# Kernel tuning notes

Measured on AMD Instinct MI355X. Metric: run time of the kernel, lower is better.

Reference implementation:

```python
import jax, jax.numpy as jnp
import numpy as np

N = 100000
E = 1600000
D_IN, H1, H2 = 64, 128, 64
ATT = 32


def _mean_aggregate(feat, src, dst, num_nodes):
    # gather source features per edge, scatter-sum to destinations, divide by in-degree
    summed = jax.ops.segment_sum(feat[src], dst, num_segments=num_nodes)  # [N, d]
    deg = jax.ops.segment_sum(jnp.ones((src.shape[0],), feat.dtype), dst, num_segments=num_nodes)
    return summed / jnp.maximum(deg, 1.0)[:, None]


def setup_inputs() -> dict:
    key = jax.random.key(0)
    ks = jax.random.split(key, 16)
    x = jax.random.normal(ks[0], (N, D_IN), dtype=jnp.float32)
    edge_index = jax.random.randint(ks[1], (2, E), 0, N, dtype=jnp.int64)

    def lin(k, fan_in, fan_out):
        bound = 1.0 / np.sqrt(fan_in)
        return jax.random.uniform(k, (fan_in, fan_out), jnp.float32, -bound, bound)

    params = {
        'W1_l': lin(ks[2], D_IN, H1), 'W1_r': lin(ks[3], D_IN, H1),
        'b1': jnp.zeros((H1,), jnp.float32),
        'W2_l': lin(ks[4], H1, H2), 'W2_r': lin(ks[5], H1, H2),
        'b2': jnp.zeros((H2,), jnp.float32),
        'Wa': lin(ks[6], H2, ATT), 'ba': jnp.zeros((ATT,), jnp.float32),
        'ctx': jax.random.normal(ks[7], (ATT,), jnp.float32),
        'Wc1': lin(ks[8], H2, H2 // 2), 'bc1': jnp.zeros((H2 // 2,), jnp.float32),
        'Wc2': lin(ks[9], H2 // 2, 1), 'bc2': jnp.zeros((1,), jnp.float32),
    }
    return {'x': x, 'edge_index': edge_index, **params}


def reference(x, edge_index, W1_l, W1_r, b1, W2_l, W2_r, b2, Wa, ba, ctx, Wc1, bc1, Wc2, bc2):
    src, dst = edge_index[0], edge_index[1]
    ionm_alerts = x[:, -1]  # [N]

    # GraphSAGE layer 1 (mean aggr): lin_l(mean_neighbors) + lin_r(x_self)
    agg1 = _mean_aggregate(x, src, dst, N)
    h = jax.nn.relu(agg1 @ W1_l + b1 + x @ W1_r)  # [N, H1]
    # F.dropout(training=False) -> identity

    # GraphSAGE layer 2
    agg2 = _mean_aggregate(h, src, dst, N)
    h = jax.nn.relu(agg2 @ W2_l + b2 + h @ W2_r)  # [N, H2]

    # attention with IONM alert boost (+0.4)
    scores = jnp.tanh(h @ Wa + ba)            # [N, ATT]
    w = scores @ ctx + ionm_alerts * 0.4       # [N]
    w = jax.nn.softmax(w, axis=0)
    h = h * w[:, None]

    pooled = jnp.mean(h, axis=0, keepdims=True)  # [1, H2]

    # classifier head (Dropout identity in eval)
    z = jax.nn.relu(pooled @ Wc1 + bc1)
    return jax.nn.sigmoid(z @ Wc2 + bc2)  # [1, 1]
```

## Files before the change

### kernel.cpp

```cpp
#include <hip/hip_runtime.h>
#include <math.h>

#define N_NODES 100000
#define E_EDGES 1600000
#define D_IN 64
#define HID1 128
#define HID2 64
#define ATT 32
#define CAP 32
#define AT_STRIDE 136
#define NRANGE 8
#define RNODES (N_NODES / NRANGE)
#define NPART 64
#define XCAST_BLOCKS ((N_NODES * 16 + 255) / 256)
#define NBLK 1024
#define EPB  1563
#define SEGCAP 384
#define SCAT2_BLOCKS 2048
#define GBLK 3125

#define SX 0.4f
#define INVSX 2.5f
#define SV 0.25f
#define INVSV 4.0f

typedef unsigned int uint32;
typedef unsigned short ushort;
typedef __attribute__((ext_vector_type(8))) short short8;
typedef __attribute__((ext_vector_type(4))) float float4v;
typedef __attribute__((ext_vector_type(2))) unsigned int uint32x2;
typedef __attribute__((ext_vector_type(4))) unsigned int uint32x4;

#define NTL(p) __builtin_nontemporal_load(&(p))

__device__ inline uint32 bf16rn(float f){ uint32 u = __float_as_uint(f); return (u + 0x7fffu + ((u >> 16) & 1u)) >> 16; }
__device__ inline uint32 packbf2(float a, float b){ return bf16rn(a) | (bf16rn(b) << 16); }

__device__ inline int swz3125(int bb){
    int x = bb & 7, k = bb >> 3;
    return (x < 5) ? x * 391 + k : 5 * 391 + (x - 5) * 390 + k;
}

#if __has_builtin(__builtin_amdgcn_sdot8)
#define HW_SDOT8 1
#endif

__device__ inline uint32 q4(float v, float inv){
    float n = rintf(v * inv);
    n = fminf(fmaxf(n, -8.f), 7.f);
    return (uint32)((int)n) & 15u;
}

__device__ inline void dec4i(uint32 w, int sh, int& a0, int& a1, int& a2, int& a3){
    a0 += ((int)(w << (28 - sh))) >> 28;
    a1 += ((int)(w << (24 - sh))) >> 28;
    a2 += ((int)(w << (20 - sh))) >> 28;
    a3 += ((int)(w << (16 - sh))) >> 28;
}

__global__ void k_mega(const float* __restrict__ x,
                       const int* __restrict__ src, const int* __restrict__ dst,
                       const float* __restrict__ W1l, const float* __restrict__ W1r,
                       const float* __restrict__ W2l, const float* __restrict__ W2r,
                       uint32* __restrict__ xb, uint32* __restrict__ xq4,
                       uint32* __restrict__ vq4, float* __restrict__ alertv,
                       ushort* __restrict__ wt1g, ushort* __restrict__ wt2g,
                       uint32x2* __restrict__ qu, int* __restrict__ qlen){
    int b = blockIdx.x, t = threadIdx.x;
    if (b < XCAST_BLOCKS){
        int i = b * 256 + t;
        if (i < N_NODES * 16){
            float4v v = NTL(((const float4v*)x)[i]);
            xb[2 * i]     = packbf2(v.x, v.y);
            xb[2 * i + 1] = packbf2(v.z, v.w);
            ((ushort*)xq4)[i] = (ushort)(q4(v.x, INVSX) | (q4(v.y, INVSX) << 4)
                              | (q4(v.z, INVSX) << 8) | (q4(v.w, INVSX) << 12));
            if ((i & 15) == 15) alertv[i >> 4] = v.w;
        }
        return;
    }
    if (b < XCAST_BLOCKS + 2){
        int sub = b - XCAST_BLOCKS;
        ushort* dstp = (sub == 0) ? wt1g : wt2g;
        for (int idx = t; idx < 128 * 128; idx += 256){
            int nn = idx >> 7, kk = idx & 127;
            float v;
            if (sub == 0) v = (kk < 64) ? W1l[kk * 128 + nn] : W1r[(kk - 64) * 128 + nn];
            else          v = (nn < 64) ? W2l[kk * 64 + nn]  : W2r[kk * 64 + (nn - 64)];
            dstp[nn * 128 + kk] = (ushort)bf16rn(v);
        }
        if (sub == 0){
            if (t < 8) xq4[(size_t)N_NODES * 8 + t] = 0u;
            else if (t < 16) vq4[(size_t)N_NODES * 8 + (t - 8)] = 0u;
        }
        return;
    }
    int blk = b - (XCAST_BLOCKS + 2);
    __shared__ int tails[NRANGE];
    if (t < NRANGE) tails[t] = 0;
    __syncthreads();
    int lane = t & 63;
    int base = blk * EPB;
    int end  = min(base + EPB, E_EDGES);
    for (int i0 = base; i0 < end; i0 += 256){
        int i = i0 + t;
        bool v = (i < end);
        int d = 0, s = 0, r = NRANGE;
        if (v){
            d = NTL(dst[i]);
            s = NTL(src[i]);
            r = (int)((uint32)d / (uint32)RNODES);
        }
        int mybase = 0, myoff = 0;
        #pragma unroll
        for (int k = 0; k < NRANGE; k++){
            unsigned long long mk = __ballot(r == k);
            if (r == k){
                int leader = (int)__ffsll((unsigned long long)mk) - 1;
                int nk = (int)__popcll(mk);
                int bse = 0;
                if (lane == leader) bse = atomicAdd(&tails[k], nk);
                bse = __shfl(bse, leader, 64);
                mybase = bse;
                myoff  = (int)__popcll(mk & ((lane == 63) ? 0x7fffffffffffffffull
                                                          : ((1ull << lane) - 1ull)));
            }
        }
        if (v){
            int pos = mybase + myoff;
            if (pos < SEGCAP)
                qu[(size_t)(blk * NRANGE + r) * SEGCAP + pos] = (uint32x2){(uint32)d, (uint32)s};
        }
    }
    __syncthreads();
    if (t < NRANGE) qlen[blk * NRANGE + t] = min(tails[t], SEGCAP);
}

__global__ __launch_bounds__(256) void k_scat2(const uint32x2* __restrict__ qu,
                                               const int* __restrict__ qlen,
                                               int* __restrict__ cnt, int* __restrict__ ssrc){
    int bb = blockIdx.x, t = threadIdx.x;
    int r = bb & (NRANGE - 1);
    int sidx = bb >> 3;
    #pragma unroll 1
    for (int k = 0; k < NBLK / (SCAT2_BLOCKS / NRANGE); k++){
        int seg = sidx * 4 + k;
        int qi = seg * NRANGE + r;
        int len = min(qlen[qi], SEGCAP);
        const uint32x2* qp = &qu[(size_t)qi * SEGCAP];
        for (int i = t; i < len; i += 256){
            uint32x2 pr = NTL(qp[i]);
            int d = (int)pr.x, s = (int)pr.y;
            int pos = atomicAdd(&cnt[d], 1);
            if (pos < CAP) ssrc[d * CAP + pos] = s;
        }
    }
}

__device__ inline void gather8_i4(const uint32* __restrict__ tab4,
                                  const int* __restrict__ ssrc,
                                  const int* __restrict__ cnt,
                                  int n0, int lane,
                                  int acc[8][4], int cct[8]){
    int q = lane >> 4, p = lane & 15;
    int dw = p >> 1, sh = (p & 1) << 4;
#ifdef HW_SDOT8
    uint32 sel0 = 1u << sh;
#endif
    int nn = n0 + (lane & 7);
    int ccl_ = cnt[nn];
    int cc[8];
    #pragma unroll
    for (int j = 0; j < 8; j++){
        int c = __shfl(ccl_, j, 64);
        cct[j] = c;
        cc[j] = min(c, CAP);
    }
    #pragma unroll
    for (int j = 0; j < 8; j++){ acc[j][0] = acc[j][1] = acc[j][2] = acc[j][3] = 0; }
    int cmax = 0;
    #pragma unroll
    for (int j = 0; j < 8; j++) cmax = max(cmax, cc[j]);
    if (cmax == 0) return;
    int se[8];
    #pragma unroll
    for (int j = 0; j < 8; j++)
        se[j] = (lane < cc[j]) ? NTL(ssrc[(n0 + j) * CAP + lane]) : N_NODES;

    uint32 w[4][8];
    #pragma unroll
    for (int g = 0; g < 4; g++){
        #pragma unroll
        for (int j = 0; j < 8; j++){
            int s = __shfl(se[j], g * 4 + q, 64);
            w[g][j] = tab4[(uint32)s * 8u + dw];
        }
    }
    #pragma unroll
    for (int g = 0; g < 4; g++){
        #pragma unroll
        for (int j = 0; j < 8; j++){
#ifdef HW_SDOT8
            acc[j][0] = __builtin_amdgcn_sdot8((int)w[g][j], (int)sel0,         acc[j][0], false);
            acc[j][1] = __builtin_amdgcn_sdot8((int)w[g][j], (int)(sel0 << 4),  acc[j][1], false);
            acc[j][2] = __builtin_amdgcn_sdot8((int)w[g][j], (int)(sel0 << 8),  acc[j][2], false);
            acc[j][3] = __builtin_amdgcn_sdot8((int)w[g][j], (int)(sel0 << 12), acc[j][3], false);
#else
            dec4i(w[g][j], sh, acc[j][0], acc[j][1], acc[j][2], acc[j][3]);
#endif
        }
    }
    if (cmax > 16){
        #pragma unroll
        for (int g = 0; g < 4; g++){
            #pragma unroll
            for (int j = 0; j < 8; j++){
                int s = __shfl(se[j], 16 + g * 4 + q, 64);
                w[g][j] = tab4[(uint32)s * 8u + dw];
            }
        }
        #pragma unroll
        for (int g = 0; g < 4; g++){
            #pragma unroll
            for (int j = 0; j < 8; j++){
#ifdef HW_SDOT8
                acc[j][0] = __builtin_amdgcn_sdot8((int)w[g][j], (int)sel0,         acc[j][0], false);
                acc[j][1] = __builtin_amdgcn_sdot8((int)w[g][j], (int)(sel0 << 4),  acc[j][1], false);
                acc[j][2] = __builtin_amdgcn_sdot8((int)w[g][j], (int)(sel0 << 8),  acc[j][2], false);
                acc[j][3] = __builtin_amdgcn_sdot8((int)w[g][j], (int)(sel0 << 12), acc[j][3], false);
#else
                dec4i(w[g][j], sh, acc[j][0], acc[j][1], acc[j][2], acc[j][3]);
#endif
            }
        }
    }
    #pragma unroll
    for (int j = 0; j < 8; j++){
        acc[j][0] += __shfl_xor(acc[j][0], 16, 64); acc[j][1] += __shfl_xor(acc[j][1], 16, 64);
        acc[j][2] += __shfl_xor(acc[j][2], 16, 64); acc[j][3] += __shfl_xor(acc[j][3], 16, 64);
        acc[j][0] += __shfl_xor(acc[j][0], 32, 64); acc[j][1] += __shfl_xor(acc[j][1], 32, 64);
        acc[j][2] += __shfl_xor(acc[j][2], 32, 64); acc[j][3] += __shfl_xor(acc[j][3], 32, 64);
    }
}

__device__ inline float inv_deg(int c){ return 1.f / fmaxf(fminf((float)c, (float)CAP), 1.f); }

__global__ __launch_bounds__(256) void k_gather(
    const uint32* __restrict__ tab4,
    const int* __restrict__ ssrc, const int* __restrict__ cnt,
    float scl, uint32* __restrict__ aggb, float* __restrict__ pzero){
    int t = threadIdx.x, wave = t >> 6, lane = t & 63;
    if (pzero != nullptr && blockIdx.x == 0){
        for (int i = t; i < NPART * 65; i += 256) pzero[i] = 0.f;
    }
    int nb0 = swz3125((int)blockIdx.x) * 32;
    int n0 = nb0 + wave * 8;
    int acc[8][4]; int cct[8];
    gather8_i4(tab4, ssrc, cnt, n0, lane, acc, cct);
    int p = lane & 15;
    if (lane < 16){
        #pragma unroll
        for (int j = 0; j < 8; j++){
            float f = scl * inv_deg(cct[j]);
            uint2 o;
            o.x = packbf2((float)acc[j][0] * f, (float)acc[j][1] * f);
            o.y = packbf2((float)acc[j][2] * f, (float)acc[j][3] * f);
            *(uint2*)&aggb[(size_t)(n0 + j) * 32 + 2 * p] = o;
        }
    }
}

__global__ __launch_bounds__(256) void k_mm(
    const uint32* __restrict__ aggb, const uint32* __restrict__ xb,
    const ushort* __restrict__ wt1g, const ushort* __restrict__ wt2g,
    const float* __restrict__ b1, const float* __restrict__ b2,
    uint32* __restrict__ vq4, ushort* __restrict__ r2b){
    __shared__ ushort smem[2 * 32 * AT_STRIDE];
    ushort* at  = smem;
    ushort* at2 = smem + 32 * AT_STRIDE;
    float* vstage = (float*)smem;
    int t = threadIdx.x, wave = t >> 6, lane = t & 63;
    int nb0 = swz3125((int)blockIdx.x) * 32;

    int m0 = t >> 3, ch = t & 7;
    uint4 aval = *(const uint4*)&aggb[(size_t)(nb0 + m0) * 32 + ch * 4];
    uint4 xval = *(const uint4*)&xb[(size_t)(nb0 + m0) * 32 + ch * 4];
    *(uint4*)((uint32*)(at + m0 * AT_STRIDE) + ch * 4) = aval;
    *(uint4*)((uint32*)(at + m0 * AT_STRIDE + 64) + ch * 4) = xval;
    __syncthreads();

    int cidx = lane & 15, quad = lane >> 4;
    int mt = wave >> 1;
    int nbase = (wave & 1) * 64;
    float4v c[4];
    #pragma unroll
    for (int nt = 0; nt < 4; nt++) c[nt] = (float4v){0.f,0.f,0.f,0.f};
    #pragma unroll
    for (int kt = 0; kt < 4; kt++){
        short8 a = *(short8*)(at + ((mt * 16 + cidx) * AT_STRIDE + kt * 32 + quad * 8));
        #pragma unroll
        for (int nt = 0; nt < 4; nt++){
            short8 b = *(const short8*)(wt1g + ((nbase + nt * 16 + cidx) * 128 + kt * 32 + quad * 8));
            c[nt] = __builtin_amdgcn_mfma_f32_16x16x32_bf16(a, b, c[nt], 0, 0, 0);
        }
    }
    #pragma unroll
    for (int nt = 0; nt < 4; nt++){
        float bb = b1[nbase + nt * 16 + cidx];
        #pragma unroll
        for (int i = 0; i < 4; i++){
            int row = quad * 4 + i;
            at2[(mt * 16 + row) * AT_STRIDE + nbase + nt * 16 + cidx] =
                (ushort)bf16rn(fmaxf(c[nt][i] + bb, 0.f));
        }
    }
    __syncthreads();
    #pragma unroll
    for (int nt = 0; nt < 4; nt++) c[nt] = (float4v){0.f,0.f,0.f,0.f};
    #pragma unroll
    for (int kt = 0; kt < 4; kt++){
        short8 a = *(short8*)(at2 + ((mt * 16 + cidx) * AT_STRIDE + kt * 32 + quad * 8));
        #pragma unroll
        for (int nt = 0; nt < 4; nt++){
            short8 b = *(const short8*)(wt2g + ((nbase + nt * 16 + cidx) * 128 + kt * 32 + quad * 8));
            c[nt] = __builtin_amdgcn_mfma_f32_16x16x32_bf16(a, b, c[nt], 0, 0, 0);
        }
    }
    if (nbase == 0){
        #pragma unroll
        for (int nt = 0; nt < 4; nt++){
            #pragma unroll
            for (int i = 0; i < 4; i++){
                int row = quad * 4 + i;
                vstage[(mt * 16 + row) * 65 + nt * 16 + cidx] = c[nt][i];
            }
        }
    } else {
        #pragma unroll
        for (int nt = 0; nt < 4; nt++){
            float bb = b2[nt * 16 + cidx];
            #pragma unroll
            for (int i = 0; i < 4; i++){
                int row = quad * 4 + i;
                size_t node = nb0 + mt * 16 + row;
                r2b[node * 64 + nt * 16 + cidx] = (ushort)bf16rn(c[nt][i] + bb);
            }
        }
    }
    __syncthreads();
    {
        int m = t >> 3, u = t & 7;
        float f0 = vstage[m * 65 + 8 * u],     f1 = vstage[m * 65 + 8 * u + 1];
        float f2 = vstage[m * 65 + 8 * u + 2], f3 = vstage[m * 65 + 8 * u + 3];
        float f4 = vstage[m * 65 + 8 * u + 4], f5 = vstage[m * 65 + 8 * u + 5];
        float f6 = vstage[m * 65 + 8 * u + 6], f7 = vstage[m * 65 + 8 * u + 7];
        vq4[(size_t)(nb0 + m) * 8 + u] =
              q4(f0, INVSV)        | (q4(f1, INVSV) << 4)  | (q4(f2, INVSV) << 8)
            | (q4(f3, INVSV) << 12)| (q4(f4, INVSV) << 16) | (q4(f5, INVSV) << 20)
            | (q4(f6, INVSV) << 24)| (q4(f7, INVSV) << 28);
    }
}

__device__ inline float bf16lo(uint32 u){ return __uint_as_float(u << 16); }
__device__ inline float bf16hi(uint32 u){ return __uint_as_float(u & 0xffff0000u); }

__global__ __launch_bounds__(256) void k_att(
    const float* __restrict__ alertv, const uint32* __restrict__ aggvb,
    const ushort* __restrict__ r2b,
    const float* __restrict__ Wa, const float* __restrict__ ba, const float* __restrict__ ctx,
    float* __restrict__ pooledP, float* __restrict__ Zpart){
    __shared__ float sh2[32][68];
    __shared__ float sew[32];
    __shared__ float sp[4][64];
    int t = threadIdx.x;
    int bn0 = swz3125((int)blockIdx.x) * 32;
    int m0 = t >> 3, ch = t & 7;
    {
        size_t nj = bn0 + m0;
        uint4 av = *(const uint4*)&aggvb[nj * 32 + ch * 4];
        uint4 rr = *(const uint4*)&r2b[nj * 64 + ch * 8];
        float4v h0, h1;
        h0.x = fmaxf(bf16lo(av.x) + bf16lo(rr.x), 0.f);
        h0.y = fmaxf(bf16hi(av.x) + bf16hi(rr.x), 0.f);
        h0.z = fmaxf(bf16lo(av.y) + bf16lo(rr.y), 0.f);
        h0.w = fmaxf(bf16hi(av.y) + bf16hi(rr.y), 0.f);
        h1.x = fmaxf(bf16lo(av.z) + bf16lo(rr.z), 0.f);
        h1.y = fmaxf(bf16hi(av.z) + bf16hi(rr.z), 0.f);
        h1.z = fmaxf(bf16lo(av.w) + bf16lo(rr.w), 0.f);
        h1.w = fmaxf(bf16hi(av.w) + bf16hi(rr.w), 0.f);
        *(float4v*)&sh2[m0][8 * ch]     = h0;
        *(float4v*)&sh2[m0][8 * ch + 4] = h1;
    }
    __syncthreads();
    int node = t >> 3;
    int c0 = (t & 7) * 4;
    float s0 = ba[c0], s1 = ba[c0 + 1], s2 = ba[c0 + 2], s3 = ba[c0 + 3];
    #pragma unroll 8
    for (int j = 0; j < 64; j++){
        float hv = sh2[node][j];
        s0 += hv * Wa[j * ATT + c0];
        s1 += hv * Wa[j * ATT + c0 + 1];
        s2 += hv * Wa[j * ATT + c0 + 2];
        s3 += hv * Wa[j * ATT + c0 + 3];
    }
    float pa = tanhf(s0) * ctx[c0] + tanhf(s1) * ctx[c0 + 1]
             + tanhf(s2) * ctx[c0 + 2] + tanhf(s3) * ctx[c0 + 3];
    #pragma unroll
    for (int off = 4; off >= 1; off >>= 1) pa += __shfl_down(pa, off, 8);
    if ((t & 7) == 0){
        int n = bn0 + node;
        float w = pa + NTL(alertv[n]) * 0.4f;
        sew[node] = expf(w);
    }
    __syncthreads();
    int j = t & 63, q = t >> 6;
    float p4 = 0.f;
    #pragma unroll
    for (int m = 0; m < 8; m++) p4 += sh2[q * 8 + m][j] * sew[q * 8 + m];
    sp[q][j] = p4;
    __syncthreads();
    if (t < 64){
        float s = sp[0][t] + sp[1][t] + sp[2][t] + sp[3][t];
        atomicAdd(&pooledP[(blockIdx.x & (NPART - 1)) * 64 + t], s);
    }
    if (t == 64){
        float z = 0.f;
        #pragma unroll
        for (int m = 0; m < 32; m++) z += sew[m];
        atomicAdd(&Zpart[blockIdx.x & (NPART - 1)], z);
    }
}

__global__ void k_final(const float* __restrict__ pooledP, const float* __restrict__ Zpart,
                        const float* __restrict__ Wc1, const float* __restrict__ bc1,
                        const float* __restrict__ Wc2, const float* __restrict__ bc2,
                        float* __restrict__ out){
    __shared__ float sp[64], sz[32];
    __shared__ float Zs;
    int t = threadIdx.x;
    float s = 0.f;
    for (int q = 0; q < NPART; q++) s += pooledP[q * 64 + t];
    if (t == 0){
        float z = 0.f;
        for (int q = 0; q < NPART; q++) z += Zpart[q];
        Zs = z;
    }
    __syncthreads();
    float scale = 1.0f / (Zs * (float)N_NODES);
    sp[t] = s * scale;
    __syncthreads();
    if (t < 32){
        float a = bc1[t];
        #pragma unroll 8
        for (int j = 0; j < 64; j++) a += sp[j] * Wc1[j * 32 + t];
        sz[t] = fmaxf(a, 0.f);
    }
    __syncthreads();
    if (t == 0){
        float a = bc2[0];
        #pragma unroll
        for (int i = 0; i < 32; i++) a += sz[i] * Wc2[i];
        out[0] = 1.0f / (1.0f + expf(-a));
    }
}

extern "C" void kernel_launch(void* const* d_in, const int* in_sizes, int n_in,
                              void* d_out, int out_size, void* d_ws, size_t ws_size,
                              hipStream_t stream) {
    const float* x   = (const float*)d_in[0];
    const int*   ei  = (const int*)d_in[1];
    const int*   src = ei;
    const int*   dst = ei + E_EDGES;
    const float* W1l = (const float*)d_in[2];
    const float* W1r = (const float*)d_in[3];
    const float* b1  = (const float*)d_in[4];
    const float* W2l = (const float*)d_in[5];
    const float* W2r = (const float*)d_in[6];
    const float* b2  = (const float*)d_in[7];
    const float* Wa  = (const float*)d_in[8];
    const float* ba  = (const float*)d_in[9];
    const float* ctx = (const float*)d_in[10];
    const float* Wc1 = (const float*)d_in[11];
    const float* bc1 = (const float*)d_in[12];
    const float* Wc2 = (const float*)d_in[13];
    const float* bc2 = (const float*)d_in[14];

    char* p = (char*)d_ws;
    int* cnt    = (int*)p;                 p += (size_t)N_NODES * 4;
    int* ssrc   = (int*)p;                 p += (size_t)N_NODES * CAP * 4;
    uint32* xb  = (uint32*)p;              p += (size_t)N_NODES * 32 * 4;
    uint32* xq4 = (uint32*)p;              p += (size_t)(N_NODES + 1) * 8 * 4;
    uint32* vq4 = (uint32*)p;              p += (size_t)(N_NODES + 1) * 8 * 4;
    char* r2region = p;                    p += (size_t)N_NODES * 64 * 4;
    ushort* wt1g = (ushort*)p;             p += 128 * 128 * 2;
    ushort* wt2g = (ushort*)p;             p += 128 * 128 * 2;
    float* pooledP = (float*)p;            p += NPART * 64 * 4;
    float* Zpart   = (float*)p;            p += NPART * 4;
    int* qlen      = (int*)p;              p += (size_t)NBLK * NRANGE * 4;
    float* alertv  = (float*)p;            p += (size_t)N_NODES * 4;
    uint32x2* qu = (uint32x2*)r2region;
    ushort* r2b  = (ushort*)r2region;
    uint32* aggb = (uint32*)(r2region + (size_t)N_NODES * 128);

    hipMemsetAsync(cnt, 0, (size_t)N_NODES * 4, stream);

    k_mega<<<XCAST_BLOCKS + 2 + NBLK, 256, 0, stream>>>(
        x, src, dst, W1l, W1r, W2l, W2r, xb, xq4, vq4, alertv, wt1g, wt2g, qu, qlen);

    k_scat2<<<SCAT2_BLOCKS, 256, 0, stream>>>(qu, qlen, cnt, ssrc);

    k_gather<<<GBLK, 256, 0, stream>>>(xq4, ssrc, cnt, SX, aggb, pooledP);
    k_mm<<<GBLK, 256, 0, stream>>>(aggb, xb, wt1g, wt2g, b1, b2, vq4, r2b);
    k_gather<<<GBLK, 256, 0, stream>>>(vq4, ssrc, cnt, SV, aggb, nullptr);
    k_att<<<GBLK, 256, 0, stream>>>(alertv, aggb, r2b, Wa, ba, ctx, pooledP, Zpart);
    k_final<<<1, 64, 0, stream>>>(pooledP, Zpart, Wc1, bc1, Wc2, bc2, (float*)d_out);
}
```

Baseline: 342.2 us.

## Replace per-node CSR build and gather with bucketed LDS-atomic aggregation

Edge binning now buckets edges into 512 destination ranges, packing the local destination and source into one word. The separate scatter kernel that built per-node source lists, and the memset of the degree counters, are removed. A new aggregation kernel runs one block per range: it reads the 4-bit source rows and accumulates them into an LDS tile with atomics, counts degrees in LDS, then writes the scaled bf16 means. This drops the global-atomic CSR pass, but the aggregation now uses only 512 blocks, one LDS atomic per lane per edge, and a small per-bucket capacity that can drop overflow edges.

```diff
diff --git a/kernel.cpp b/kernel.cpp
--- a/kernel.cpp
+++ b/kernel.cpp
@@ -7,16 +7,14 @@
 #define HID1 128
 #define HID2 64
 #define ATT 32
-#define CAP 32
 #define AT_STRIDE 136
-#define NRANGE 8
-#define RNODES (N_NODES / NRANGE)
 #define NPART 64
 #define XCAST_BLOCKS ((N_NODES * 16 + 255) / 256)
-#define NBLK 1024
-#define EPB  1563
-#define SEGCAP 384
-#define SCAT2_BLOCKS 2048
+#define NBLK 256
+#define EPB  6250
+#define NR   512
+#define RSUB 196
+#define SEGCAP 32
 #define GBLK 3125
 
 #define SX 0.4f
@@ -28,8 +26,6 @@
 typedef unsigned short ushort;
 typedef __attribute__((ext_vector_type(8))) short short8;
 typedef __attribute__((ext_vector_type(4))) float float4v;
-typedef __attribute__((ext_vector_type(2))) unsigned int uint32x2;
-typedef __attribute__((ext_vector_type(4))) unsigned int uint32x4;
 
 #define NTL(p) __builtin_nontemporal_load(&(p))
 
@@ -40,22 +36,11 @@
     int x = bb & 7, k = bb >> 3;
     return (x < 5) ? x * 391 + k : 5 * 391 + (x - 5) * 390 + k;
 }
-
-#if __has_builtin(__builtin_amdgcn_sdot8)
-#define HW_SDOT8 1
-#endif
 
 __device__ inline uint32 q4(float v, float inv){
     float n = rintf(v * inv);
     n = fminf(fmaxf(n, -8.f), 7.f);
     return (uint32)((int)n) & 15u;
-}
-
-__device__ inline void dec4i(uint32 w, int sh, int& a0, int& a1, int& a2, int& a3){
-    a0 += ((int)(w << (28 - sh))) >> 28;
-    a1 += ((int)(w << (24 - sh))) >> 28;
-    a2 += ((int)(w << (20 - sh))) >> 28;
-    a3 += ((int)(w << (16 - sh))) >> 28;
 }
 
 __global__ void k_mega(const float* __restrict__ x,
@@ -63,9 +48,9 @@
                        const float* __restrict__ W1l, const float* __restrict__ W1r,
                        const float* __restrict__ W2l, const float* __restrict__ W2r,
                        uint32* __restrict__ xb, uint32* __restrict__ xq4,
-                       uint32* __restrict__ vq4, float* __restrict__ alertv,
+                       float* __restrict__ alertv,
                        ushort* __restrict__ wt1g, ushort* __restrict__ wt2g,
-                       uint32x2* __restrict__ qu, int* __restrict__ qlen){
+                       uint32* __restrict__ qu, int* __restrict__ qlen){
     int b = blockIdx.x, t = threadIdx.x;
     if (b < XCAST_BLOCKS){
         int i = b * 256 + t;
@@ -89,183 +74,80 @@
             else          v = (nn < 64) ? W2l[kk * 64 + nn]  : W2r[kk * 64 + (nn - 64)];
             dstp[nn * 128 + kk] = (ushort)bf16rn(v);
         }
-        if (sub == 0){
-            if (t < 8) xq4[(size_t)N_NODES * 8 + t] = 0u;
-            else if (t < 16) vq4[(size_t)N_NODES * 8 + (t - 8)] = 0u;
-        }
         return;
     }
     int blk = b - (XCAST_BLOCKS + 2);
-    __shared__ int tails[NRANGE];
-    if (t < NRANGE) tails[t] = 0;
-    __syncthreads();
-    int lane = t & 63;
+    __shared__ int tails[NR];
+    for (int k = t; k < NR; k += 256) tails[k] = 0;
+    __syncthreads();
     int base = blk * EPB;
     int end  = min(base + EPB, E_EDGES);
-    for (int i0 = base; i0 < end; i0 += 256){
-        int i = i0 + t;
-        bool v = (i < end);
-        int d = 0, s = 0, r = NRANGE;
-        if (v){
-            d = NTL(dst[i]);
-            s = NTL(src[i]);
-            r = (int)((uint32)d / (uint32)RNODES);
-        }
-        int mybase = 0, myoff = 0;
-        #pragma unroll
-        for (int k = 0; k < NRANGE; k++){
-            unsigned long long mk = __ballot(r == k);
-            if (r == k){
-                int leader = (int)__ffsll((unsigned long long)mk) - 1;
-                int nk = (int)__popcll(mk);
-                int bse = 0;
-                if (lane == leader) bse = atomicAdd(&tails[k], nk);
-                bse = __shfl(bse, leader, 64);
-                mybase = bse;
-                myoff  = (int)__popcll(mk & ((lane == 63) ? 0x7fffffffffffffffull
-                                                          : ((1ull << lane) - 1ull)));
+    for (int i = base + t; i < end; i += 256){
+        int d = NTL(dst[i]);
+        int s = NTL(src[i]);
+        uint32 r = (uint32)d / (uint32)RSUB;
+        uint32 dloc = (uint32)d - r * (uint32)RSUB;
+        int pos = atomicAdd(&tails[r], 1);
+        if (pos < SEGCAP)
+            qu[(size_t)((uint32)blk * NR + r) * SEGCAP + pos] = (dloc << 17) | (uint32)s;
+    }
+    __syncthreads();
+    for (int k = t; k < NR; k += 256) qlen[blk * NR + k] = min(tails[k], SEGCAP);
+}
+
+__global__ __launch_bounds__(256) void k_agg(
+    const uint32* __restrict__ tab4, const uint32* __restrict__ qu,
+    const int* __restrict__ qlen, float scl,
+    uint32* __restrict__ aggb, float* __restrict__ pzero){
+    __shared__ int accl[RSUB * 64];
+    __shared__ int cntl[RSUB];
+    int t = threadIdx.x, wave = t >> 6, lane = t & 63;
+    int r = blockIdx.x;
+    if (pzero != nullptr && r == 0){
+        for (int i = t; i < NPART * 65; i += 256) pzero[i] = 0.f;
+    }
+    for (int i = t; i < RSUB * 64; i += 256) accl[i] = 0;
+    for (int i = t; i < RSUB; i += 256) cntl[i] = 0;
+    __syncthreads();
+    int dwi = lane >> 3;
+    int sh  = (lane & 7) << 2;
+    for (int bb = wave; bb < NBLK; bb += 4){
+        int qi = bb * NR + r;
+        int len = min(qlen[qi], SEGCAP);
+        if (len == 0) continue;
+        const uint32* qp = &qu[(size_t)qi * SEGCAP];
+        uint32 pk = (lane < len) ? NTL(qp[lane]) : 0u;
+        for (int base = 0; base < len; base += 8){
+            int m = len - base;
+            uint32 wv[8]; int dl[8];
+            #pragma unroll
+            for (int k = 0; k < 8; k++){
+                if (k < m){
+                    uint32 p2 = (uint32)__shfl((int)pk, base + k, 64);
+                    dl[k] = (int)(p2 >> 17);
+                    wv[k] = tab4[(p2 & 0x1FFFFu) * 8u + dwi];
+                }
             }
-        }
-        if (v){
-            int pos = mybase + myoff;
-            if (pos < SEGCAP)
-                qu[(size_t)(blk * NRANGE + r) * SEGCAP + pos] = (uint32x2){(uint32)d, (uint32)s};
-        }
-    }
-    __syncthreads();
-    if (t < NRANGE) qlen[blk * NRANGE + t] = min(tails[t], SEGCAP);
-}
-
-__global__ __launch_bounds__(256) void k_scat2(const uint32x2* __restrict__ qu,
-                                               const int* __restrict__ qlen,
-                                               int* __restrict__ cnt, int* __restrict__ ssrc){
-    int bb = blockIdx.x, t = threadIdx.x;
-    int r = bb & (NRANGE - 1);
-    int sidx = bb >> 3;
-    #pragma unroll 1
-    for (int k = 0; k < NBLK / (SCAT2_BLOCKS / NRANGE); k++){
-        int seg = sidx * 4 + k;
-        int qi = seg * NRANGE + r;
-        int len = min(qlen[qi], SEGCAP);
-        const uint32x2* qp = &qu[(size_t)qi * SEGCAP];
-        for (int i = t; i < len; i += 256){
-            uint32x2 pr = NTL(qp[i]);
-            int d = (int)pr.x, s = (int)pr.y;
-            int pos = atomicAdd(&cnt[d], 1);
-            if (pos < CAP) ssrc[d * CAP + pos] = s;
-        }
-    }
-}
-
-__device__ inline void gather8_i4(const uint32* __restrict__ tab4,
-                                  const int* __restrict__ ssrc,
-                                  const int* __restrict__ cnt,
-                                  int n0, int lane,
-                                  int acc[8][4], int cct[8]){
-    int q = lane >> 4, p = lane & 15;
-    int dw = p >> 1, sh = (p & 1) << 4;
-#ifdef HW_SDOT8
-    uint32 sel0 = 1u << sh;
-#endif
-    int nn = n0 + (lane & 7);
-    int ccl_ = cnt[nn];
-    int cc[8];
-    #pragma unroll
-    for (int j = 0; j < 8; j++){
-        int c = __shfl(ccl_, j, 64);
-        cct[j] = c;
-        cc[j] = min(c, CAP);
-    }
-    #pragma unroll
-    for (int j = 0; j < 8; j++){ acc[j][0] = acc[j][1] = acc[j][2] = acc[j][3] = 0; }
-    int cmax = 0;
-    #pragma unroll
-    for (int j = 0; j < 8; j++) cmax = max(cmax, cc[j]);
-    if (cmax == 0) return;
-    int se[8];
-    #pragma unroll
-    for (int j = 0; j < 8; j++)
-        se[j] = (lane < cc[j]) ? NTL(ssrc[(n0 + j) * CAP + lane]) : N_NODES;
-
-    uint32 w[4][8];
-    #pragma unroll
-    for (int g = 0; g < 4; g++){
-        #pragma unroll
-        for (int j = 0; j < 8; j++){
-            int s = __shfl(se[j], g * 4 + q, 64);
-            w[g][j] = tab4[(uint32)s * 8u + dw];
-        }
-    }
-    #pragma unroll
-    for (int g = 0; g < 4; g++){
-        #pragma unroll
-        for (int j = 0; j < 8; j++){
-#ifdef HW_SDOT8
-            acc[j][0] = __builtin_amdgcn_sdot8((int)w[g][j], (int)sel0,         acc[j][0], false);
-            acc[j][1] = __builtin_amdgcn_sdot8((int)w[g][j], (int)(sel0 << 4),  acc[j][1], false);
-            acc[j][2] = __builtin_amdgcn_sdot8((int)w[g][j], (int)(sel0 << 8),  acc[j][2], false);
-            acc[j][3] = __builtin_amdgcn_sdot8((int)w[g][j], (int)(sel0 << 12), acc[j][3], false);
-#else
-            dec4i(w[g][j], sh, acc[j][0], acc[j][1], acc[j][2], acc[j][3]);
-#endif
-        }
-    }
-    if (cmax > 16){
-        #pragma unroll
-        for (int g = 0; g < 4; g++){
             #pragma unroll
-            for (int j = 0; j < 8; j++){
-                int s = __shfl(se[j], 16 + g * 4 + q, 64);
-                w[g][j] = tab4[(uint32)s * 8u + dw];
+            for (int k = 0; k < 8; k++){
+                if (k < m){
+                    int v = ((int)(wv[k] << (28 - sh))) >> 28;
+                    atomicAdd(&accl[dl[k] * 64 + lane], v);
+                    if (lane == 0) atomicAdd(&cntl[dl[k]], 1);
+                }
             }
         }
-        #pragma unroll
-        for (int g = 0; g < 4; g++){
-            #pragma unroll
-            for (int j = 0; j < 8; j++){
-#ifdef HW_SDOT8
-                acc[j][0] = __builtin_amdgcn_sdot8((int)w[g][j], (int)sel0,         acc[j][0], false);
-                acc[j][1] = __builtin_amdgcn_sdot8((int)w[g][j], (int)(sel0 << 4),  acc[j][1], false);
-                acc[j][2] = __builtin_amdgcn_sdot8((int)w[g][j], (int)(sel0 << 8),  acc[j][2], false);
-                acc[j][3] = __builtin_amdgcn_sdot8((int)w[g][j], (int)(sel0 << 12), acc[j][3], false);
-#else
-                dec4i(w[g][j], sh, acc[j][0], acc[j][1], acc[j][2], acc[j][3]);
-#endif
-            }
-        }
-    }
-    #pragma unroll
-    for (int j = 0; j < 8; j++){
-        acc[j][0] += __shfl_xor(acc[j][0], 16, 64); acc[j][1] += __shfl_xor(acc[j][1], 16, 64);
-        acc[j][2] += __shfl_xor(acc[j][2], 16, 64); acc[j][3] += __shfl_xor(acc[j][3], 16, 64);
-        acc[j][0] += __shfl_xor(acc[j][0], 32, 64); acc[j][1] += __shfl_xor(acc[j][1], 32, 64);
-        acc[j][2] += __shfl_xor(acc[j][2], 32, 64); acc[j][3] += __shfl_xor(acc[j][3], 32, 64);
-    }
-}
-
-__device__ inline float inv_deg(int c){ return 1.f / fmaxf(fminf((float)c, (float)CAP), 1.f); }
-
-__global__ __launch_bounds__(256) void k_gather(
-    const uint32* __restrict__ tab4,
-    const int* __restrict__ ssrc, const int* __restrict__ cnt,
-    float scl, uint32* __restrict__ aggb, float* __restrict__ pzero){
-    int t = threadIdx.x, wave = t >> 6, lane = t & 63;
-    if (pzero != nullptr && blockIdx.x == 0){
-        for (int i = t; i < NPART * 65; i += 256) pzero[i] = 0.f;
-    }
-    int nb0 = swz3125((int)blockIdx.x) * 32;
-    int n0 = nb0 + wave * 8;
-    int acc[8][4]; int cct[8];
-    gather8_i4(tab4, ssrc, cnt, n0, lane, acc, cct);
-    int p = lane & 15;
-    if (lane < 16){
-        #pragma unroll
-        for (int j = 0; j < 8; j++){
-            float f = scl * inv_deg(cct[j]);
-            uint2 o;
-            o.x = packbf2((float)acc[j][0] * f, (float)acc[j][1] * f);
-            o.y = packbf2((float)acc[j][2] * f, (float)acc[j][3] * f);
-            *(uint2*)&aggb[(size_t)(n0 + j) * 32 + 2 * p] = o;
+    }
+    __syncthreads();
+    int nbase = r * RSUB;
+    for (int i = t; i < RSUB * 32; i += 256){
+        int n = i >> 5, dp = i & 31;
+        int gn = nbase + n;
+        if (gn < N_NODES){
+            float f = scl / fmaxf((float)cntl[n], 1.f);
+            aggb[(size_t)gn * 32 + dp] =
+                packbf2((float)accl[n * 64 + 2 * dp] * f,
+                        (float)accl[n * 64 + 2 * dp + 1] * f);
         }
     }
 }
@@ -486,32 +368,25 @@
     const float* bc2 = (const float*)d_in[14];
 
     char* p = (char*)d_ws;
-    int* cnt    = (int*)p;                 p += (size_t)N_NODES * 4;
-    int* ssrc   = (int*)p;                 p += (size_t)N_NODES * CAP * 4;
     uint32* xb  = (uint32*)p;              p += (size_t)N_NODES * 32 * 4;
     uint32* xq4 = (uint32*)p;              p += (size_t)(N_NODES + 1) * 8 * 4;
     uint32* vq4 = (uint32*)p;              p += (size_t)(N_NODES + 1) * 8 * 4;
-    char* r2region = p;                    p += (size_t)N_NODES * 64 * 4;
+    uint32* qu  = (uint32*)p;              p += (size_t)NBLK * NR * SEGCAP * 4;
+    int* qlen   = (int*)p;                 p += (size_t)NBLK * NR * 4;
+    ushort* r2b = (ushort*)p;              p += (size_t)N_NODES * 64 * 2;
+    uint32* aggb = (uint32*)p;             p += (size_t)N_NODES * 32 * 4;
     ushort* wt1g = (ushort*)p;             p += 128 * 128 * 2;
     ushort* wt2g = (ushort*)p;             p += 128 * 128 * 2;
     float* pooledP = (float*)p;            p += NPART * 64 * 4;
     float* Zpart   = (float*)p;            p += NPART * 4;
-    int* qlen      = (int*)p;              p += (size_t)NBLK * NRANGE * 4;
     float* alertv  = (float*)p;            p += (size_t)N_NODES * 4;
-    uint32x2* qu = (uint32x2*)r2region;
-    ushort* r2b  = (ushort*)r2region;
-    uint32* aggb = (uint32*)(r2region + (size_t)N_NODES * 128);
-
-    hipMemsetAsync(cnt, 0, (size_t)N_NODES * 4, stream);
 
     k_mega<<<XCAST_BLOCKS + 2 + NBLK, 256, 0, stream>>>(
-        x, src, dst, W1l, W1r, W2l, W2r, xb, xq4, vq4, alertv, wt1g, wt2g, qu, qlen);
-
-    k_scat2<<<SCAT2_BLOCKS, 256, 0, stream>>>(qu, qlen, cnt, ssrc);
-
-    k_gather<<<GBLK, 256, 0, stream>>>(xq4, ssrc, cnt, SX, aggb, pooledP);
+        x, src, dst, W1l, W1r, W2l, W2r, xb, xq4, alertv, wt1g, wt2g, qu, qlen);
+
+    k_agg<<<NR, 256, 0, stream>>>(xq4, qu, qlen, SX, aggb, pooledP);
     k_mm<<<GBLK, 256, 0, stream>>>(aggb, xb, wt1g, wt2g, b1, b2, vq4, r2b);
-    k_gather<<<GBLK, 256, 0, stream>>>(vq4, ssrc, cnt, SV, aggb, nullptr);
+    k_agg<<<NR, 256, 0, stream>>>(vq4, qu, qlen, SV, aggb, nullptr);
     k_att<<<GBLK, 256, 0, stream>>>(alertv, aggb, r2b, Wa, ba, ctx, pooledP, Zpart);
     k_final<<<1, 64, 0, stream>>>(pooledP, Zpart, Wc1, bc1, Wc2, bc2, (float*)d_out);
 }
```

New measurement: 775.8 us. 2.27x slower.
